# Kernel optimization log

Measured on AMD Instinct MI355X. Metric: run time of the kernel, lower is better.

The kernel has to match this reference:

```python
import jax, jax.numpy as jnp
import numpy as np

B, NQ, DM = 2, 8192, 256
NH, DH, NL, NP = 6, 64, 3, 9
IMG_H, IMG_W = 384, 1280
SHAPES = [(48, 160), (24, 80), (12, 40)]  # (h, w) per pyramid level


def setup_inputs() -> dict:
    key = jax.random.key(0)
    ks = jax.random.split(key, 16)
    inp = {}
    inp["x"] = jax.random.normal(ks[0], (B, NQ, DM), jnp.float32)
    inp["pe"] = jax.random.normal(ks[1], (B, NQ, DM), jnp.float32)
    # lidar points in front of the camera so projected uv mostly lands in-image
    u = jax.random.uniform(ks[2], (B, NQ, 3), jnp.float32)
    inp["coor"] = jnp.stack([(u[..., 0] - 0.5) * 40.0,
                             (u[..., 1] - 0.5) * 4.0,
                             2.0 + u[..., 2] * 48.0], axis=-1)
    K = jnp.array([[700., 0., 640., 0.], [0., 700., 192., 0.],
                   [0., 0., 1., 0.], [0., 0., 0., 1.]], jnp.float32)
    inp["cam2img"] = jnp.broadcast_to(K, (B, 4, 4))
    inp["lidar2cam"] = jnp.broadcast_to(jnp.eye(4, dtype=jnp.float32), (B, 4, 4))
    for i, (h, w) in enumerate(SHAPES):
        inp[f"feat{i}"] = jax.random.normal(ks[3 + i], (B, DM, h, w), jnp.float32) * 0.1
    s = 1.0 / np.sqrt(DM).astype(np.float32)
    inp["W_value"] = jax.random.normal(ks[6], (DM, NH * DH), jnp.float32) * s
    inp["b_value"] = jnp.zeros((NH * DH,), jnp.float32)
    inp["W_off"] = jax.random.normal(ks[7], (DM, NH * NL * NP * 2), jnp.float32) * 0.01
    inp["b_off"] = jax.random.normal(ks[8], (NH * NL * NP * 2,), jnp.float32)
    inp["W_attn"] = jax.random.normal(ks[9], (DM, NH * NL * NP), jnp.float32) * s
    inp["b_attn"] = jnp.zeros((NH * NL * NP,), jnp.float32)
    inp["W_out"] = jax.random.normal(ks[10], (NH * DH, DM), jnp.float32) * (1.0 / np.sqrt(NH * DH)).astype(np.float32)
    inp["b_out"] = jnp.zeros((DM,), jnp.float32)
    return inp


def _points2uv(points, cam2img, lidar2cam):
    R, t = lidar2cam[:, :3, :3], lidar2cam[:, :3, 3]
    pc = jnp.einsum('bij,bnj->bni', R, points) + t[:, None, :]
    Kr, Kt = cam2img[:, :3, :3], cam2img[:, :3, 3]
    p2 = jnp.einsum('bij,bnj->bni', Kr, pc) + Kt[:, None, :]
    return p2[..., :2] / p2[..., 2:3]  # [B,NQ,2] (u,v)


def _bilinear_gather(v, loc, hl, wl):
    # v: [B*NH, hl*wl, DH] values; loc: [B,NQ,NH,NP,2] normalized [0,1]
    # matches grid_sample(bilinear, padding=zeros, align_corners=False)
    x = loc[..., 0] * wl - 0.5
    y = loc[..., 1] * hl - 0.5
    x0 = jnp.floor(x)
    y0 = jnp.floor(y)
    fx = x - x0
    fy = y - y0
    acc = jnp.zeros((B, NH, NQ, NP, DH), v.dtype)
    for dy in (0, 1):
        for dx in (0, 1):
            xi = x0 + dx
            yi = y0 + dy
            wgt = (fx if dx else 1.0 - fx) * (fy if dy else 1.0 - fy)
            valid = (xi >= 0) & (xi < wl) & (yi >= 0) & (yi < hl)
            idx = (jnp.clip(yi, 0, hl - 1) * wl + jnp.clip(xi, 0, wl - 1)).astype(jnp.int32)
            idx = idx.transpose(0, 2, 1, 3).reshape(B * NH, NQ * NP)
            g = jax.vmap(lambda vt, it: vt[it])(v, idx)  # [B*NH, NQ*NP, DH]
            g = g.reshape(B, NH, NQ, NP, DH)
            wv = (wgt * valid).transpose(0, 2, 1, 3)      # [B,NH,NQ,NP]
            acc = acc + g * wv[..., None]
    return acc


def reference(x, pe, coor, cam2img, lidar2cam, feat0, feat1, feat2,
              W_value, b_value, W_off, b_off, W_attn, b_attn, W_out, b_out):
    feats = [feat0, feat1, feat2]
    uv = _points2uv(coor, cam2img, lidar2cam)  # [B,NQ,2]
    # per-level reference points in level pixel coords: uv * (w_l/W, h_l/H)
    ref = jnp.stack([uv * jnp.array([w / IMG_W, h / IMG_H], jnp.float32)
                     for (h, w) in SHAPES], axis=2)  # [B,NQ,NL,2]
    q = x + pe
    off = (q @ W_off + b_off).reshape(B, NQ, NH, NL, NP, 2)
    attn = jax.nn.softmax((q @ W_attn + b_attn).reshape(B, NQ, NH, NL * NP), axis=-1)
    attn = attn.reshape(B, NQ, NH, NL, NP).transpose(0, 2, 1, 3, 4)  # [B,NH,NQ,NL,NP]
    norm = jnp.array([[w, h] for (h, w) in SHAPES], jnp.float32)     # [NL,2] (w,h)
    loc = (ref[:, :, None, :, None, :] + off) / norm[None, None, None, :, None, :]
    out = jnp.zeros((B, NH, NQ, DH), jnp.float32)
    for l, (h, w) in enumerate(SHAPES):
        src = feats[l].reshape(B, DM, h * w).transpose(0, 2, 1)  # [B,hw,DM]
        v = (src @ W_value + b_value).reshape(B, h * w, NH, DH)
        v = v.transpose(0, 2, 1, 3).reshape(B * NH, h * w, DH)
        sampled = _bilinear_gather(v, loc[:, :, :, l], h, w)    # [B,NH,NQ,NP,DH]
        out = out + jnp.einsum('bhqp,bhqpd->bhqd', attn[:, :, :, l], sampled)
    out = out.transpose(0, 2, 1, 3).reshape(B, NQ, NH * DH)
    return out @ W_out + b_out  # dropout is identity at eval
```

## Files before the change

kernel.cpp:

```cpp
#include <hip/hip_runtime.h>
#include <hip/hip_bf16.h>
#include <hip/hip_fp16.h>

#define NQ_   8192
#define DM_   256
#define NH_   6
#define DH_   64
#define BATCH 2

typedef __attribute__((ext_vector_type(8))) short short8;
typedef __attribute__((ext_vector_type(4))) short short4v;
typedef __attribute__((ext_vector_type(4))) float float4v;
typedef __attribute__((ext_vector_type(2))) float f32x2;
typedef __attribute__((ext_vector_type(4))) unsigned int uint32x4;
typedef __attribute__((ext_vector_type(4))) int int32x4;

#if defined(__has_builtin)
#if __has_builtin(__builtin_amdgcn_make_buffer_rsrc) && __has_builtin(__builtin_amdgcn_raw_ptr_buffer_load_b128)
#define USE_BUFLD 1
#endif
#endif
#ifndef USE_BUFLD
#define USE_BUFLD 0
#endif

static const size_t VOFF_L0 = 0;
static const size_t VOFF_L1 = 5898240;
static const size_t VOFF_L2 = 7372800;
static const size_t QRAW_BYTE_OFF  = 15482880;
static const size_t MID_BYTE_OFF   = 47333376;
static const size_t QBF_BYTE_OFF   = 47333376;
static const size_t WT_BYTE_OFF    = 59916288;
static const size_t FEATT_BYTE_OFF = 60558336;
static const size_t REF_BYTE_OFF   = 70880256;
static const size_t WVT_OFF   = 0;
static const size_t WOFFT_OFF = 98304;
static const size_t WATTN_OFF = 181248;
static const size_t WOUTT_OFF = 222720;
static const size_t FT_L0 = 0;
static const size_t FT_L1 = 3932160;
static const size_t FT_L2 = 4915200;

__device__ __forceinline__ unsigned short f2bf(float f) {
    unsigned int u = __float_as_uint(f);
    unsigned int r = (u + 0x7fffu + ((u >> 16) & 1u)) >> 16;
    return (unsigned short)r;
}

__device__ __forceinline__ void cp16(void* lds, const void* g) {
    __builtin_amdgcn_global_load_lds(
        (const __attribute__((address_space(1))) unsigned int*)g,
        (__attribute__((address_space(3))) unsigned int*)lds, 16, 0, 0);
}

__device__ __forceinline__ void fm_lo(float& acc, float w, unsigned d) {
    asm("v_fma_mix_f32 %0, %1, %2, %0 op_sel:[0,0,0] op_sel_hi:[0,1,0]"
        : "+v"(acc) : "v"(w), "v"(d));
}
__device__ __forceinline__ void fm_hi(float& acc, float w, unsigned d) {
    asm("v_fma_mix_f32 %0, %1, %2, %0 op_sel:[0,1,0] op_sel_hi:[0,1,0]"
        : "+v"(acc) : "v"(w), "v"(d));
}

__global__ __launch_bounds__(256) void prep_all(const float* __restrict__ Wv,
                                                const float* __restrict__ Woff,
                                                const float* __restrict__ Wattn,
                                                const float* __restrict__ Wout,
                                                const float* __restrict__ feat0,
                                                const float* __restrict__ feat1,
                                                const float* __restrict__ feat2,
                                                const float* __restrict__ x,
                                                const float* __restrict__ pe,
                                                const float* __restrict__ coor,
                                                const float* __restrict__ cam2img,
                                                const float* __restrict__ l2c,
                                                unsigned short* __restrict__ wT,
                                                unsigned short* __restrict__ fT,
                                                unsigned short* __restrict__ qbf,
                                                float* __restrict__ ref) {
    const int pid = blockIdx.x, t = threadIdx.x;
    if (pid < 84) {
        __shared__ float tile[64][65];
        int r = pid;
        const float* src; int K, N, nt, kt; size_t base;
        if (r < 24)      { src = Wv;    K = 256; N = 384; nt = r >> 2; kt = r & 3; base = WVT_OFF; }
        else if (r < 48) { r -= 24; src = Woff;  K = 256; N = 324; nt = r >> 2; kt = r & 3; base = WOFFT_OFF; }
        else if (r < 60) { r -= 48; src = Wattn; K = 256; N = 162; nt = r >> 2; kt = r & 3; base = WATTN_OFF; }
        else             { r -= 60; src = Wout;  K = 384; N = 256; nt = r / 6;  kt = r % 6; base = WOUTT_OFF; }
        const int n0 = nt * 64, k0t = kt * 64;
        {
            int nl = t & 63, kl4 = t >> 6;
            int nn = min(n0 + nl, N - 1);
#pragma unroll
            for (int i = 0; i < 16; ++i) {
                int kl = kl4 + i * 4;
                tile[nl][kl] = src[(size_t)(k0t + kl) * N + nn];
            }
        }
        __syncthreads();
        {
            int kl = t & 63, nl4 = t >> 6;
#pragma unroll
            for (int i = 0; i < 16; ++i) {
                int nl = nl4 + i * 4;
                if (n0 + nl < N)
                    wT[base + (size_t)(n0 + nl) * K + k0t + kl] = f2bf(tile[nl][kl]);
            }
        }
        return;
    }
    if (pid < 2604) {
        __shared__ float tile[64][33];
        int f = pid - 84;
        const float* src; unsigned short* dst; int HW;
        if (f < 1920)      { src = feat0; dst = fT + FT_L0; HW = 7680; }
        else if (f < 2400) { src = feat1; dst = fT + FT_L1; HW = 1920; f -= 1920; }
        else               { src = feat2; dst = fT + FT_L2; HW = 480;  f -= 2400; }
        int pb = f >> 3, rem = f & 7, cb = rem >> 1, b = rem & 1;
        int p0 = pb * 32, c0 = cb * 64;
        {
            int px = t & 31, cy = t >> 5;
#pragma unroll
            for (int i = 0; i < 8; ++i) {
                int cr = cy + i * 8;
                tile[cr][px] = src[((size_t)(b * DM_ + c0 + cr)) * HW + p0 + px];
            }
        }
        __syncthreads();
        {
            int cx = t & 63, py = t >> 6;
#pragma unroll
            for (int i = 0; i < 8; ++i) {
                int pr = py + i * 4;
                dst[((size_t)b * HW + p0 + pr) * DM_ + c0 + cx] = f2bf(tile[cx][pr]);
            }
        }
        return;
    }
    if (pid < 3628) {
        int f = pid - 2604;
#pragma unroll
        for (int i = 0; i < 4; ++i) {
            size_t e = (size_t)f * 4096 + i * 1024 + t * 4;
            float4 xv = *(const float4*)&x[e];
            float4 pv = *(const float4*)&pe[e];
            short4v o;
            o[0] = (short)f2bf(xv.x + pv.x);
            o[1] = (short)f2bf(xv.y + pv.y);
            o[2] = (short)f2bf(xv.z + pv.z);
            o[3] = (short)f2bf(xv.w + pv.w);
            *(short4v*)&qbf[e] = o;
        }
        return;
    }
    {
        int q = (pid - 3628) * 256 + t;
        int b = q >> 13;
        float c0 = coor[(size_t)q * 3 + 0];
        float c1 = coor[(size_t)q * 3 + 1];
        float c2 = coor[(size_t)q * 3 + 2];
        const float* L = l2c + b * 16;
        const float* C = cam2img + b * 16;
        float pc0 = L[0] * c0 + L[1] * c1 + L[2]  * c2 + L[3];
        float pc1 = L[4] * c0 + L[5] * c1 + L[6]  * c2 + L[7];
        float pc2 = L[8] * c0 + L[9] * c1 + L[10] * c2 + L[11];
        float q0 = C[0] * pc0 + C[1] * pc1 + C[2]  * pc2 + C[3];
        float q1 = C[4] * pc0 + C[5] * pc1 + C[6]  * pc2 + C[7];
        float q2 = C[8] * pc0 + C[9] * pc1 + C[10] * pc2 + C[11];
        float rz = __frcp_rn(q2);
        float rx = q0 * rz * 0.125f, ry = q1 * rz * 0.125f;
#pragma unroll
        for (int l = 0; l < 3; ++l) {
            float sl = (l == 0) ? 1.f : ((l == 1) ? 0.5f : 0.25f);
            f32x2 v = {rx * sl - 0.5f, ry * sl - 0.5f};
            *(f32x2*)&ref[(size_t)q * 6 + l * 2] = v;
        }
    }
}

__device__ __forceinline__ void mfma_block64(const short A[][64], const short B[][64],
                                             int wm, int wn, int lane, float4v acc[4][4]) {
    int mb = wm + (lane & 15);
    int nb = wn + (lane & 15);
    int q8 = (lane >> 4) * 8;
#pragma unroll
    for (int kk = 0; kk < 2; ++kk) {
        short8 af[4], bf[4];
#pragma unroll
        for (int i = 0; i < 4; ++i) {
            int m = mb + i * 16;
            af[i] = *(const short8*)&A[m][(q8 + kk * 32) ^ ((m & 7) * 8)];
        }
#pragma unroll
        for (int j = 0; j < 4; ++j) {
            int n = nb + j * 16;
            bf[j] = *(const short8*)&B[n][(q8 + kk * 32) ^ ((n & 7) * 8)];
        }
#pragma unroll
        for (int i = 0; i < 4; ++i)
#pragma unroll
            for (int j = 0; j < 4; ++j)
                acc[i][j] = __builtin_amdgcn_mfma_f32_16x16x32_bf16(af[i], bf[j], acc[i][j], 0, 0, 0);
    }
}

__global__ __launch_bounds__(256) void gemm_vq(const unsigned short* __restrict__ fT,
                                               const unsigned short* __restrict__ wT,
                                               const float* __restrict__ bv,
                                               unsigned short* __restrict__ vws,
                                               const unsigned short* __restrict__ qbf,
                                               const float* __restrict__ boff,
                                               const float* __restrict__ battn,
                                               float* __restrict__ qraw) {
    __shared__ short A[128][64];
    __shared__ short B[128][64];
    const int tid = threadIdx.x;
    const int lane = tid & 63, wave = tid >> 6;
    const int wm = (wave & 1) * 64, wn = (wave >> 1) * 64;
    const int id = blockIdx.x;
    const int sr = tid >> 3;
    const int sc8 = (tid & 7) * 8;
    const int scsw = (((tid & 7) ^ (sr & 7)) * 8);
    float4v acc[4][4];
#pragma unroll
    for (int i = 0; i < 4; ++i)
#pragma unroll
        for (int j = 0; j < 4; ++j) acc[i][j] = (float4v){0.f, 0.f, 0.f, 0.f};

    if (id < 474) {
        int pb = id / 6, rem = id % 6;
        int nb = rem >> 1, b = rem & 1;
        int pbl, HW; size_t ftoff, voff;
        if (pb < 60)      { pbl = pb;      HW = 7680; ftoff = FT_L0; voff = VOFF_L0; }
        else if (pb < 75) { pbl = pb - 60; HW = 1920; ftoff = FT_L1; voff = VOFF_L1; }
        else              { pbl = pb - 75; HW = 480;  ftoff = FT_L2; voff = VOFF_L2; }
        const int p0 = pbl * 128, n0 = nb * 128;
        const unsigned short* Asrc = fT + ftoff + (size_t)b * HW * DM_;
        const unsigned short* wvT = wT + WVT_OFF;
        int prow[4];
#pragma unroll
        for (int i = 0; i < 4; ++i) { int p = p0 + sr + 32 * i; prow[i] = min(p, HW - 1); }

        for (int k0 = 0; k0 < DM_; k0 += 64) {
#pragma unroll
            for (int i = 0; i < 4; ++i)
                cp16(&A[sr + 32 * i][sc8], &Asrc[(size_t)prow[i] * DM_ + k0 + scsw]);
#pragma unroll
            for (int i = 0; i < 4; ++i)
                cp16(&B[sr + 32 * i][sc8], &wvT[(size_t)(n0 + sr + 32 * i) * DM_ + k0 + scsw]);
            __syncthreads();
            mfma_block64(A, B, wm, wn, lane, acc);
            __syncthreads();
        }
        int colb = n0 + wn + (lane & 15);
        int rowq = (lane >> 4) * 4;
#pragma unroll
        for (int i = 0; i < 4; ++i)
#pragma unroll
            for (int j = 0; j < 4; ++j) {
                int n = colb + j * 16;
                int h = n >> 6, d = n & 63;
                float bias = bv[n];
#pragma unroll
                for (int r = 0; r < 4; ++r) {
                    int p = p0 + wm + i * 16 + rowq + r;
                    if (p < HW)
                        vws[voff + ((size_t)(b * NH_ + h) * HW + p) * DH_ + d] =
                            __half_as_ushort(__float2half(acc[i][j][r] + bias));
                }
            }
    } else {
        int qid = id - 474;
        const int m0 = (qid & 127) * 128, n0 = (qid >> 7) * 128;
        const unsigned short* wq = wT + WOFFT_OFF;

        for (int k0 = 0; k0 < DM_; k0 += 64) {
#pragma unroll
            for (int i = 0; i < 4; ++i)
                cp16(&A[sr + 32 * i][sc8], &qbf[(size_t)(m0 + sr + 32 * i) * DM_ + k0 + scsw]);
#pragma unroll
            for (int i = 0; i < 4; ++i)
                cp16(&B[sr + 32 * i][sc8], &wq[(size_t)(n0 + sr + 32 * i) * DM_ + k0 + scsw]);
            __syncthreads();
            mfma_block64(A, B, wm, wn, lane, acc);
            __syncthreads();
        }
        int colb = n0 + wn + (lane & 15);
        int rowq = (lane >> 4) * 4;
#pragma unroll
        for (int i = 0; i < 4; ++i)
#pragma unroll
            for (int j = 0; j < 4; ++j) {
                int n = colb + j * 16;
                if (n < 486) {
                    float bias = (n < 324) ? boff[n] : battn[n - 324];
#pragma unroll
                    for (int r = 0; r < 4; ++r) {
                        int m = m0 + wm + i * 16 + rowq + r;
                        qraw[(size_t)m * 486 + n] = acc[i][j][r] + bias;
                    }
                }
            }
    }
}

template<int N>
__device__ __forceinline__ void gather_batch(const int2* __restrict__ pl, int t0, unsigned cb,
#if USE_BUFLD
                                             __amdgpu_buffer_rsrc_t vrs,
#else
                                             const char* vbase,
#endif
                                             float (&a)[8]) {
    int2 pw[N];
    uint32x4 d[N];
#pragma unroll
    for (int t = 0; t < N; ++t) pw[t] = pl[t0 + t];
#pragma unroll
    for (int t = 0; t < N; ++t) {
#if USE_BUFLD
        int32x4 t4 = __builtin_amdgcn_raw_ptr_buffer_load_b128(
            vrs, (int)((unsigned)pw[t].x + cb), 0, 0);
        d[t] = __builtin_bit_cast(uint32x4, t4);
#else
        d[t] = *(const uint32x4*)(vbase + ((unsigned)pw[t].x + cb));
#endif
    }
#pragma unroll
    for (int t = 0; t < N; ++t) {
        float w = __int_as_float(pw[t].y);
        fm_lo(a[0], w, d[t][0]); fm_hi(a[1], w, d[t][0]);
        fm_lo(a[2], w, d[t][1]); fm_hi(a[3], w, d[t][1]);
        fm_lo(a[4], w, d[t][2]); fm_hi(a[5], w, d[t][2]);
        fm_lo(a[6], w, d[t][3]); fm_hi(a[7], w, d[t][3]);
    }
}

__global__ __launch_bounds__(192, 6) void sample_kernel(const float* __restrict__ qraw,
                                                        const float* __restrict__ ref,
                                                        const unsigned short* __restrict__ vws,
                                                        unsigned short* __restrict__ mid) {
    __shared__ int2 s_plan[792];
    const int tid = threadIdx.x;
    const int bq = blockIdx.x;
    const int b = bq >> 13;
    int ntq;

    {
        int h = tid >> 5, j = tid & 31;
        bool act = j < 27;
        float logit = act ? qraw[(size_t)bq * 486 + 324 + h * 27 + j] : -1e30f;
        float m = logit;
#pragma unroll
        for (int msk = 16; msk >= 1; msk >>= 1) m = fmaxf(m, __shfl_xor(m, msk, 32));
        float e = act ? __expf(logit - m) : 0.f;
        float ssum = e;
#pragma unroll
        for (int msk = 16; msk >= 1; msk >>= 1) ssum += __shfl_xor(ssum, msk, 32);

        bool keep = false;
        int off0 = 0, off1 = 0;
        float p00 = 0.f, p01 = 0.f, p10 = 0.f, p11 = 0.f;
        if (act) {
            float attn = e * __frcp_rn(ssum);
            int l = (j >= 18) ? 2 : ((j >= 9) ? 1 : 0);
            int wl = 160 >> l, hl = 48 >> l;
            int HWl = (l == 0) ? 7680 : ((l == 1) ? 1920 : 480);
            int lvlb = (l == 0) ? 0 : ((l == 1) ? 11796480 : 14745600);
            f32x2 r2 = *(const f32x2*)&ref[(size_t)bq * 6 + l * 2];
            float2 oxy = *(const float2*)&qraw[(size_t)bq * 486 + h * 54 + j * 2];
            float X = r2[0] + oxy.x;
            float Y = r2[1] + oxy.y;
            float x0f = floorf(X), y0f = floorf(Y);
            float fx = X - x0f, fy = Y - y0f;
            int ix = (int)x0f, iy = (int)y0f;
            int bx = min(max(ix, 0), wl - 2);
            float wx0 = ((bx == ix) ? (1.f - fx) : 0.f) + ((bx == ix + 1) ? fx : 0.f);
            float wx1 = ((bx + 1 == ix) ? (1.f - fx) : 0.f) + ((bx + 1 == ix + 1) ? fx : 0.f);
            int cy0 = min(max(iy, 0), hl - 1);
            int cy1 = min(max(iy + 1, 0), hl - 1);
            float wy0 = (iy >= 0 && iy < hl) ? (1.f - fy) : 0.f;
            float wy1 = (iy + 1 >= 0 && iy + 1 < hl) ? fy : 0.f;
            keep = ((wy0 + wy1) * (wx0 + wx1)) != 0.f;
            int slice = (b * NH_ + h) * HWl;
            off0 = lvlb + (slice + cy0 * wl + bx) * 128;
            off1 = lvlb + (slice + cy1 * wl + bx) * 128;
            p00 = attn * wy0 * wx0;
            p01 = attn * wy0 * wx1;
            p10 = attn * wy1 * wx0;
            p11 = attn * wy1 * wx1;
        }
        unsigned long long mask = __ballot(keep);
        unsigned lo32 = (unsigned)mask, hi32 = (unsigned)(mask >> 32);
        bool upper = (tid & 32) != 0;
        unsigned gmask = upper ? hi32 : lo32;
        unsigned omask = upper ? lo32 : hi32;
        int slot = __popc(gmask & ((1u << j) - 1));
        int cn = __popc(gmask);
        ntq = max(cn, __popc(omask));
        ntq = ((ntq + 2) / 3) * 3;
        if (keep) {
            s_plan[(0 * 6 + h) * 33 + slot] = make_int2(off0,       __float_as_int(p00));
            s_plan[(1 * 6 + h) * 33 + slot] = make_int2(off0 + 128, __float_as_int(p01));
            s_plan[(2 * 6 + h) * 33 + slot] = make_int2(off1,       __float_as_int(p10));
            s_plan[(3 * 6 + h) * 33 + slot] = make_int2(off1 + 128, __float_as_int(p11));
        }
        if (j >= cn && j < ntq) {
            int2 z = make_int2(0, 0);
            s_plan[(0 * 6 + h) * 33 + j] = z;
            s_plan[(1 * 6 + h) * 33 + j] = z;
            s_plan[(2 * 6 + h) * 33 + j] = z;
            s_plan[(3 * 6 + h) * 33 + j] = z;
        }
    }
    __syncthreads();

    const int h = tid >> 5;
    const int l32 = tid & 31;
    const int corner = l32 >> 3;
    const unsigned cb = (unsigned)((l32 & 7) << 4);
    const int2* pl = &s_plan[(corner * 6 + h) * 33];
    float a[8] = {0.f, 0.f, 0.f, 0.f, 0.f, 0.f, 0.f, 0.f};

#if USE_BUFLD
    __amdgpu_buffer_rsrc_t vrs = __builtin_amdgcn_make_buffer_rsrc(
        const_cast<unsigned short*>(vws), (short)0, 15482880, 0x00020000);
#define VARG vrs
#else
    const char* vbase = (const char*)vws;
#define VARG vbase
#endif

    int t0 = 0;
    for (; t0 + 9 <= ntq; t0 += 9) gather_batch<9>(pl, t0, cb, VARG, a);
    for (; t0 < ntq; t0 += 3)      gather_batch<3>(pl, t0, cb, VARG, a);

#pragma unroll
    for (int i = 0; i < 8; ++i) {
        a[i] += __shfl_xor(a[i], 8, 64);
        a[i] += __shfl_xor(a[i], 16, 64);
    }
    if (corner == 0) {
        uint4 pk;
        pk.x = (unsigned)f2bf(a[0]) | ((unsigned)f2bf(a[1]) << 16);
        pk.y = (unsigned)f2bf(a[2]) | ((unsigned)f2bf(a[3]) << 16);
        pk.z = (unsigned)f2bf(a[4]) | ((unsigned)f2bf(a[5]) << 16);
        pk.w = (unsigned)f2bf(a[6]) | ((unsigned)f2bf(a[7]) << 16);
        *(uint4*)&mid[(size_t)bq * 384 + h * DH_ + ((l32 & 7) << 3)] = pk;
    }
}

__global__ __launch_bounds__(256) void out_gemm(const unsigned short* __restrict__ mid,
                                                const unsigned short* __restrict__ woT,
                                                const float* __restrict__ bout,
                                                float* __restrict__ out) {
    __shared__ short A[64][64];
    __shared__ short B[128][64];
    const int tid = threadIdx.x;
    const int m0 = blockIdx.x * 64, n0 = blockIdx.y * 128;
    const int lane = tid & 63, wave = tid >> 6;
    const int wn = wave * 32;
    const int sr = tid >> 3;
    const int sc8 = (tid & 7) * 8;
    const int scsw = (((tid & 7) ^ (sr & 7)) * 8);
    float4v acc[4][2];
#pragma unroll
    for (int i = 0; i < 4; ++i)
#pragma unroll
        for (int j = 0; j < 2; ++j) acc[i][j] = (float4v){0.f, 0.f, 0.f, 0.f};

    for (int k0 = 0; k0 < 384; k0 += 64) {
#pragma unroll
        for (int i = 0; i < 2; ++i)
            cp16(&A[sr + 32 * i][sc8], &mid[(size_t)(m0 + sr + 32 * i) * 384 + k0 + scsw]);
#pragma unroll
        for (int i = 0; i < 4; ++i)
            cp16(&B[sr + 32 * i][sc8], &woT[(size_t)(n0 + sr + 32 * i) * 384 + k0 + scsw]);
        __syncthreads();
        {
            int mb = lane & 15;
            int nb = wn + (lane & 15);
            int q8 = (lane >> 4) * 8;
#pragma unroll
            for (int kk = 0; kk < 2; ++kk) {
                short8 af[4], bf[2];
#pragma unroll
                for (int i = 0; i < 4; ++i) {
                    int m = mb + i * 16;
                    af[i] = *(const short8*)&A[m][(q8 + kk * 32) ^ ((m & 7) * 8)];
                }
#pragma unroll
                for (int j = 0; j < 2; ++j) {
                    int n = nb + j * 16;
                    bf[j] = *(const short8*)&B[n][(q8 + kk * 32) ^ ((n & 7) * 8)];
                }
#pragma unroll
                for (int i = 0; i < 4; ++i)
#pragma unroll
                    for (int j = 0; j < 2; ++j)
                        acc[i][j] = __builtin_amdgcn_mfma_f32_16x16x32_bf16(af[i], bf[j], acc[i][j], 0, 0, 0);
            }
        }
        __syncthreads();
    }
    int colb = n0 + wn + (lane & 15);
    int rowq = (lane >> 4) * 4;
#pragma unroll
    for (int i = 0; i < 4; ++i)
#pragma unroll
        for (int j = 0; j < 2; ++j) {
            int n = colb + j * 16;
            float bias = bout[n];
#pragma unroll
            for (int r = 0; r < 4; ++r) {
                int m = m0 + i * 16 + rowq + r;
                out[(size_t)m * 256 + n] = acc[i][j][r] + bias;
            }
        }
}

extern "C" void kernel_launch(void* const* d_in, const int* in_sizes, int n_in,
                              void* d_out, int out_size, void* d_ws, size_t ws_size,
                              hipStream_t stream) {
    const float* x      = (const float*)d_in[0];
    const float* pe     = (const float*)d_in[1];
    const float* coor   = (const float*)d_in[2];
    const float* c2i    = (const float*)d_in[3];
    const float* l2c    = (const float*)d_in[4];
    const float* feat0  = (const float*)d_in[5];
    const float* feat1  = (const float*)d_in[6];
    const float* feat2  = (const float*)d_in[7];
    const float* Wv     = (const float*)d_in[8];
    const float* bv     = (const float*)d_in[9];
    const float* Woff   = (const float*)d_in[10];
    const float* boff   = (const float*)d_in[11];
    const float* Wattn  = (const float*)d_in[12];
    const float* battn  = (const float*)d_in[13];
    const float* Wout   = (const float*)d_in[14];
    const float* bout   = (const float*)d_in[15];

    unsigned short* vws = (unsigned short*)d_ws;
    float* qraw         = (float*)((char*)d_ws + QRAW_BYTE_OFF);
    unsigned short* mid = (unsigned short*)((char*)d_ws + MID_BYTE_OFF);
    unsigned short* qbf = (unsigned short*)((char*)d_ws + QBF_BYTE_OFF);
    unsigned short* wT  = (unsigned short*)((char*)d_ws + WT_BYTE_OFF);
    unsigned short* fT  = (unsigned short*)((char*)d_ws + FEATT_BYTE_OFF);
    float* ref          = (float*)((char*)d_ws + REF_BYTE_OFF);
    float* out          = (float*)d_out;

    prep_all<<<dim3(3692), 256, 0, stream>>>(Wv, Woff, Wattn, Wout, feat0, feat1, feat2,
                                             x, pe, coor, c2i, l2c, wT, fT, qbf, ref);
    gemm_vq<<<dim3(986), 256, 0, stream>>>(fT, wT, bv, vws, qbf, boff, battn, qraw);
    sample_kernel<<<dim3(BATCH * NQ_), 192, 0, stream>>>(qraw, ref, vws, mid);
    out_gemm<<<dim3(256, 2), 256, 0, stream>>>(mid, wT + WOUTT_OFF, bout, out);
}
```

Before: 202.2 us.

## Process eight queries per sample block with prefetch and no block barrier

The sampling kernel now loops over eight consecutive queries per block instead of launching one block per query. While one query's gathers run, the next query's logits, offsets and reference points are loaded ahead. Each head's plan is written and read by threads of the same wave, so the block-wide barrier is removed. This cuts block launch and setup cost, but leaves far fewer blocks in the grid, which risks lower occupancy, less latency hiding across waves, and a tail effect.

```diff
diff --git a/kernel.cpp b/kernel.cpp
--- a/kernel.cpp
+++ b/kernel.cpp
@@ -342,14 +342,37 @@
                                                         unsigned short* __restrict__ mid) {
     __shared__ int2 s_plan[792];
     const int tid = threadIdx.x;
-    const int bq = blockIdx.x;
-    const int b = bq >> 13;
-    int ntq;
-
-    {
-        int h = tid >> 5, j = tid & 31;
-        bool act = j < 27;
-        float logit = act ? qraw[(size_t)bq * 486 + 324 + h * 27 + j] : -1e30f;
+    const int h = tid >> 5, j = tid & 31;
+    const bool act = j < 27;
+    const int l = (j >= 18) ? 2 : ((j >= 9) ? 1 : 0);
+    const int corner = j >> 3;
+    const unsigned cb = (unsigned)((j & 7) << 4);
+    const int2* pl = &s_plan[(corner * 6 + h) * 33];
+
+#if USE_BUFLD
+    __amdgpu_buffer_rsrc_t vrs = __builtin_amdgcn_make_buffer_rsrc(
+        const_cast<unsigned short*>(vws), (short)0, 15482880, 0x00020000);
+#define VARG vrs
+#else
+    const char* vbase = (const char*)vws;
+#define VARG vbase
+#endif
+
+    int bq = blockIdx.x * 8;
+    float plog = act ? qraw[(size_t)bq * 486 + 324 + h * 27 + j] : -1e30f;
+    float2 poxy = make_float2(0.f, 0.f);
+    f32x2 pr2 = {0.f, 0.f};
+    if (act) {
+        poxy = *(const float2*)&qraw[(size_t)bq * 486 + h * 54 + j * 2];
+        pr2  = *(const f32x2*)&ref[(size_t)bq * 6 + l * 2];
+    }
+
+    for (int it = 0; it < 8; ++it, ++bq) {
+        const int b = bq >> 13;
+        const float logit = plog;
+        const float2 oxy = poxy;
+        const f32x2 r2 = pr2;
+
         float m = logit;
 #pragma unroll
         for (int msk = 16; msk >= 1; msk >>= 1) m = fmaxf(m, __shfl_xor(m, msk, 32));
@@ -363,12 +386,9 @@
         float p00 = 0.f, p01 = 0.f, p10 = 0.f, p11 = 0.f;
         if (act) {
             float attn = e * __frcp_rn(ssum);
-            int l = (j >= 18) ? 2 : ((j >= 9) ? 1 : 0);
             int wl = 160 >> l, hl = 48 >> l;
             int HWl = (l == 0) ? 7680 : ((l == 1) ? 1920 : 480);
             int lvlb = (l == 0) ? 0 : ((l == 1) ? 11796480 : 14745600);
-            f32x2 r2 = *(const f32x2*)&ref[(size_t)bq * 6 + l * 2];
-            float2 oxy = *(const float2*)&qraw[(size_t)bq * 486 + h * 54 + j * 2];
             float X = r2[0] + oxy.x;
             float Y = r2[1] + oxy.y;
             float x0f = floorf(X), y0f = floorf(Y);
@@ -397,7 +417,7 @@
         unsigned omask = upper ? lo32 : hi32;
         int slot = __popc(gmask & ((1u << j) - 1));
         int cn = __popc(gmask);
-        ntq = max(cn, __popc(omask));
+        int ntq = max(cn, __popc(omask));
         ntq = ((ntq + 2) / 3) * 3;
         if (keep) {
             s_plan[(0 * 6 + h) * 33 + slot] = make_int2(off0,       __float_as_int(p00));
@@ -412,41 +432,34 @@
             s_plan[(2 * 6 + h) * 33 + j] = z;
             s_plan[(3 * 6 + h) * 33 + j] = z;
         }
-    }
-    __syncthreads();
-
-    const int h = tid >> 5;
-    const int l32 = tid & 31;
-    const int corner = l32 >> 3;
-    const unsigned cb = (unsigned)((l32 & 7) << 4);
-    const int2* pl = &s_plan[(corner * 6 + h) * 33];
-    float a[8] = {0.f, 0.f, 0.f, 0.f, 0.f, 0.f, 0.f, 0.f};
-
-#if USE_BUFLD
-    __amdgpu_buffer_rsrc_t vrs = __builtin_amdgcn_make_buffer_rsrc(
-        const_cast<unsigned short*>(vws), (short)0, 15482880, 0x00020000);
-#define VARG vrs
-#else
-    const char* vbase = (const char*)vws;
-#define VARG vbase
-#endif
-
-    int t0 = 0;
-    for (; t0 + 9 <= ntq; t0 += 9) gather_batch<9>(pl, t0, cb, VARG, a);
-    for (; t0 < ntq; t0 += 3)      gather_batch<3>(pl, t0, cb, VARG, a);
-
-#pragma unroll
-    for (int i = 0; i < 8; ++i) {
-        a[i] += __shfl_xor(a[i], 8, 64);
-        a[i] += __shfl_xor(a[i], 16, 64);
-    }
-    if (corner == 0) {
-        uint4 pk;
-        pk.x = (unsigned)f2bf(a[0]) | ((unsigned)f2bf(a[1]) << 16);
-        pk.y = (unsigned)f2bf(a[2]) | ((unsigned)f2bf(a[3]) << 16);
-        pk.z = (unsigned)f2bf(a[4]) | ((unsigned)f2bf(a[5]) << 16);
-        pk.w = (unsigned)f2bf(a[6]) | ((unsigned)f2bf(a[7]) << 16);
-        *(uint4*)&mid[(size_t)bq * 384 + h * DH_ + ((l32 & 7) << 3)] = pk;
+
+        if (it < 7) {
+            int bqn = bq + 1;
+            plog = act ? qraw[(size_t)bqn * 486 + 324 + h * 27 + j] : -1e30f;
+            if (act) {
+                poxy = *(const float2*)&qraw[(size_t)bqn * 486 + h * 54 + j * 2];
+                pr2  = *(const f32x2*)&ref[(size_t)bqn * 6 + l * 2];
+            }
+        }
+
+        float a[8] = {0.f, 0.f, 0.f, 0.f, 0.f, 0.f, 0.f, 0.f};
+        int t0 = 0;
+        for (; t0 + 9 <= ntq; t0 += 9) gather_batch<9>(pl, t0, cb, VARG, a);
+        for (; t0 < ntq; t0 += 3)      gather_batch<3>(pl, t0, cb, VARG, a);
+
+#pragma unroll
+        for (int i = 0; i < 8; ++i) {
+            a[i] += __shfl_xor(a[i], 8, 64);
+            a[i] += __shfl_xor(a[i], 16, 64);
+        }
+        if (corner == 0) {
+            uint4 pk;
+            pk.x = (unsigned)f2bf(a[0]) | ((unsigned)f2bf(a[1]) << 16);
+            pk.y = (unsigned)f2bf(a[2]) | ((unsigned)f2bf(a[3]) << 16);
+            pk.z = (unsigned)f2bf(a[4]) | ((unsigned)f2bf(a[5]) << 16);
+            pk.w = (unsigned)f2bf(a[6]) | ((unsigned)f2bf(a[7]) << 16);
+            *(uint4*)&mid[(size_t)bq * 384 + h * DH_ + ((j & 7) << 3)] = pk;
+        }
     }
 }
 
@@ -551,6 +564,6 @@
     prep_all<<<dim3(3692), 256, 0, stream>>>(Wv, Woff, Wattn, Wout, feat0, feat1, feat2,
                                              x, pe, coor, c2i, l2c, wT, fT, qbf, ref);
     gemm_vq<<<dim3(986), 256, 0, stream>>>(fT, wT, bv, vws, qbf, boff, battn, qraw);
-    sample_kernel<<<dim3(BATCH * NQ_), 192, 0, stream>>>(qraw, ref, vws, mid);
+    sample_kernel<<<dim3(BATCH * NQ_ / 8), 192, 0, stream>>>(qraw, ref, vws, mid);
     out_gemm<<<dim3(256, 2), 256, 0, stream>>>(mid, wT + WOUTT_OFF, bout, out);
 }
```

Result: slower. 212.4 us (+5.0%).
